# Kernel optimization log

Measured on AMD Instinct MI355X. Metric: run time of the kernel, lower is better.

## Reference

```python
import jax, jax.numpy as jnp
import numpy as np

GAMMA = 2.0
MARGIN = 0.3
SCALE = 30.0
B, C = 4096, 32768


def setup_inputs() -> dict:
    key = jax.random.key(0)
    k1, k2 = jax.random.split(key)
    inputs = jax.random.normal(k1, (B, C), dtype=jnp.float32)
    targets = jax.random.randint(k2, (B,), 0, C, dtype=jnp.int64)
    return {"inputs": inputs, "targets": targets}


def reference(inputs, targets):
    # Row-wise L2 normalize (F.normalize with eps=1e-12)
    norm = jnp.maximum(jnp.linalg.norm(inputs, axis=1, keepdims=True), 1e-12)
    normalized = inputs / norm  # (B, C)

    rows = jnp.arange(inputs.shape[0])
    # cos(theta) at target class
    cos_theta = normalized[rows, targets]
    theta = jnp.arccos(jnp.clip(cos_theta, -1.0 + 1e-7, 1.0 - 1e-7))
    cos_theta_m = jnp.cos(theta + MARGIN)

    # scatter margin-adjusted cosine back, then scale
    logits = normalized.at[rows, targets].set(cos_theta_m) * SCALE  # (B, C)

    # cross-entropy (no smoothing, no class weights)
    logp = jax.nn.log_softmax(logits, axis=1)
    ce = -logp[rows, targets]  # (B,)

    pt = jnp.exp(-ce)
    loss = (1.0 - pt) ** GAMMA * ce
    return jnp.mean(loss)
```

## Files before the change

### kernel.cpp

```cpp
#include <hip/hip_runtime.h>
#include <math.h>

#define B_ROWS 4096
#define C_COLS 32768
#define BLOCK  1024
#define NF4    (C_COLS / 4 / BLOCK)

typedef float v4f __attribute__((ext_vector_type(4)));

__device__ __forceinline__ float wave_reduce_sum(float v) {
    #pragma unroll
    for (int off = 32; off > 0; off >>= 1)
        v += __shfl_down(v, off, 64);
    return v;
}

__device__ __forceinline__ float block_reduce_sum(float v, float* red, int tid) {
    const int wid  = tid >> 6;
    const int lane = tid & 63;
    v = wave_reduce_sum(v);
    if (lane == 0) red[wid] = v;
    __syncthreads();
    if (wid == 0) {
        float s = (lane < 16) ? red[lane] : 0.0f;
        #pragma unroll
        for (int off = 8; off > 0; off >>= 1)
            s += __shfl_down(s, off, 64);
        if (lane == 0) red[0] = s;
    }
    __syncthreads();
    return red[0];
}

__global__ __launch_bounds__(BLOCK, 8)
void focal_row_kernel(const float* __restrict__ inp,
                      const int*   __restrict__ tgt,
                      float*       __restrict__ row_loss) {
    constexpr float SCALE = 30.0f;
    constexpr float COSM  = 0.9553364891f;
    constexpr float SINM  = 0.2955202067f;

    const int row = blockIdx.x;
    const int tid = threadIdx.x;

    const v4f* __restrict__ rowp = (const v4f*)(inp + (size_t)row * C_COLS);

    __shared__ float red_a[16];
    __shared__ float red_b[16];

    float xt = 0.0f;
    if (tid == 0) {
        const int ct = tgt[row];
        xt = inp[(size_t)row * C_COLS + ct];
    }

    v4f r[NF4];
    #pragma unroll
    for (int k = 0; k < NF4; ++k)
        r[k] = __builtin_nontemporal_load(rowp + (k * BLOCK + tid));

    float sumsq = 0.0f;
    #pragma unroll
    for (int k = 0; k < NF4; ++k) {
        sumsq = fmaf(r[k].x, r[k].x, sumsq);
        sumsq = fmaf(r[k].y, r[k].y, sumsq);
        sumsq = fmaf(r[k].z, r[k].z, sumsq);
        sumsq = fmaf(r[k].w, r[k].w, sumsq);
    }

    const float total_sq = block_reduce_sum(sumsq, red_a, tid);
    const float norm = fmaxf(sqrtf(total_sq), 1e-12f);
    const float inv  = SCALE / norm;

    float se = 0.0f;
    #pragma unroll
    for (int k = 0; k < NF4; ++k) {
        se += __expf(r[k].x * inv);
        se += __expf(r[k].y * inv);
        se += __expf(r[k].z * inv);
        se += __expf(r[k].w * inv);
    }
    const float sumexp_full = block_reduce_sum(se, red_b, tid);

    if (tid == 0) {
        const float c  = xt / norm;
        const float cc = fminf(fmaxf(c, -1.0f + 1e-7f), 1.0f - 1e-7f);
        const float sin_t = sqrtf(fmaxf(1.0f - cc * cc, 0.0f));
        const float cosm  = cc * COSM - sin_t * SINM;
        const float lt    = SCALE * cosm;

        const float Z  = sumexp_full - __expf(SCALE * c) + __expf(lt);
        const float ce = logf(Z) - lt;
        const float pt = __expf(-ce);
        const float om = 1.0f - pt;
        row_loss[row] = om * om * ce;
    }
}

__global__ __launch_bounds__(1024)
void finalize_kernel(const float* __restrict__ row_loss,
                     float*       __restrict__ out) {
    const int tid = threadIdx.x;
    __shared__ float red[16];
    float s = 0.0f;
    #pragma unroll
    for (int k = 0; k < B_ROWS / 1024; ++k)
        s += row_loss[k * 1024 + tid];
    const float total = block_reduce_sum(s, red, tid);
    if (tid == 0) out[0] = total * (1.0f / (float)B_ROWS);
}

extern "C" void kernel_launch(void* const* d_in, const int* in_sizes, int n_in,
                              void* d_out, int out_size, void* d_ws, size_t ws_size,
                              hipStream_t stream) {
    const float* inp = (const float*)d_in[0];
    const int*   tgt = (const int*)d_in[1];
    float*       out = (float*)d_out;
    float*       row_loss = (float*)d_ws;

    focal_row_kernel<<<B_ROWS, BLOCK, 0, stream>>>(inp, tgt, row_loss);
    finalize_kernel<<<1, 1024, 0, stream>>>(row_loss, out);
}
```

Measured before the change: 639.6 us.

## Make row kernel persistent with double-buffered next-row prefetch and LDS-only barriers

The grid shrinks to 256 blocks, and each block walks 16 consecutive rows. While the current row is reduced, the next row is loaded into a second register buffer. Barriers now wait only on LDS counters (lgkmcnt) rather than a full __syncthreads, so the in-flight global prefetch loads are not drained at each reduction. The aim is to hide memory latency behind the exp/reduction work and cut block launch overhead. The cost is lower occupancy (one 1024-thread block per CU with the launch bound relaxed to 4), higher register pressure, and dependence on a hand-encoded waitcnt value.

```diff
diff --git a/kernel.cpp b/kernel.cpp
--- a/kernel.cpp
+++ b/kernel.cpp
@@ -5,8 +5,15 @@
 #define C_COLS 32768
 #define BLOCK  1024
 #define NF4    (C_COLS / 4 / BLOCK)
+#define GRID   256
+#define RPB    (B_ROWS / GRID)
 
 typedef float v4f __attribute__((ext_vector_type(4)));
+
+__device__ __forceinline__ void bar_lds() {
+    __builtin_amdgcn_s_waitcnt(0xC07F);
+    __builtin_amdgcn_s_barrier();
+}
 
 __device__ __forceinline__ float wave_reduce_sum(float v) {
     #pragma unroll
@@ -20,7 +27,7 @@
     const int lane = tid & 63;
     v = wave_reduce_sum(v);
     if (lane == 0) red[wid] = v;
-    __syncthreads();
+    bar_lds();
     if (wid == 0) {
         float s = (lane < 16) ? red[lane] : 0.0f;
         #pragma unroll
@@ -28,11 +35,11 @@
             s += __shfl_down(s, off, 64);
         if (lane == 0) red[0] = s;
     }
-    __syncthreads();
+    bar_lds();
     return red[0];
 }
 
-__global__ __launch_bounds__(BLOCK, 8)
+__global__ __launch_bounds__(BLOCK, 4)
 void focal_row_kernel(const float* __restrict__ inp,
                       const int*   __restrict__ tgt,
                       float*       __restrict__ row_loss) {
@@ -40,60 +47,75 @@
     constexpr float COSM  = 0.9553364891f;
     constexpr float SINM  = 0.2955202067f;
 
-    const int row = blockIdx.x;
-    const int tid = threadIdx.x;
-
-    const v4f* __restrict__ rowp = (const v4f*)(inp + (size_t)row * C_COLS);
+    const int tid  = threadIdx.x;
+    const int row0 = blockIdx.x * RPB;
 
     __shared__ float red_a[16];
     __shared__ float red_b[16];
 
+    v4f buf[2][NF4];
+
+    {
+        const v4f* __restrict__ p = (const v4f*)(inp + (size_t)row0 * C_COLS);
+        #pragma unroll
+        for (int k = 0; k < NF4; ++k)
+            buf[0][k] = __builtin_nontemporal_load(p + (k * BLOCK + tid));
+    }
     float xt = 0.0f;
-    if (tid == 0) {
-        const int ct = tgt[row];
-        xt = inp[(size_t)row * C_COLS + ct];
-    }
+    if (tid == 0) xt = inp[(size_t)row0 * C_COLS + tgt[row0]];
 
-    v4f r[NF4];
-    #pragma unroll
-    for (int k = 0; k < NF4; ++k)
-        r[k] = __builtin_nontemporal_load(rowp + (k * BLOCK + tid));
+    #pragma unroll 2
+    for (int i = 0; i < RPB; ++i) {
+        const int row = row0 + i;
+        v4f* cur = buf[i & 1];
+        v4f* nxt = buf[(i + 1) & 1];
 
-    float sumsq = 0.0f;
-    #pragma unroll
-    for (int k = 0; k < NF4; ++k) {
-        sumsq = fmaf(r[k].x, r[k].x, sumsq);
-        sumsq = fmaf(r[k].y, r[k].y, sumsq);
-        sumsq = fmaf(r[k].z, r[k].z, sumsq);
-        sumsq = fmaf(r[k].w, r[k].w, sumsq);
-    }
+        float sumsq = 0.0f;
+        #pragma unroll
+        for (int k = 0; k < NF4; ++k) {
+            sumsq = fmaf(cur[k].x, cur[k].x, sumsq);
+            sumsq = fmaf(cur[k].y, cur[k].y, sumsq);
+            sumsq = fmaf(cur[k].z, cur[k].z, sumsq);
+            sumsq = fmaf(cur[k].w, cur[k].w, sumsq);
+        }
 
-    const float total_sq = block_reduce_sum(sumsq, red_a, tid);
-    const float norm = fmaxf(sqrtf(total_sq), 1e-12f);
-    const float inv  = SCALE / norm;
+        float xt_next = 0.0f;
+        if (i + 1 < RPB) {
+            const v4f* __restrict__ p = (const v4f*)(inp + (size_t)(row + 1) * C_COLS);
+            #pragma unroll
+            for (int k = 0; k < NF4; ++k)
+                nxt[k] = __builtin_nontemporal_load(p + (k * BLOCK + tid));
+            if (tid == 0) xt_next = inp[(size_t)(row + 1) * C_COLS + tgt[row + 1]];
+        }
 
-    float se = 0.0f;
-    #pragma unroll
-    for (int k = 0; k < NF4; ++k) {
-        se += __expf(r[k].x * inv);
-        se += __expf(r[k].y * inv);
-        se += __expf(r[k].z * inv);
-        se += __expf(r[k].w * inv);
-    }
-    const float sumexp_full = block_reduce_sum(se, red_b, tid);
+        const float total_sq = block_reduce_sum(sumsq, red_a, tid);
+        const float norm = fmaxf(sqrtf(total_sq), 1e-12f);
+        const float inv  = SCALE / norm;
 
-    if (tid == 0) {
-        const float c  = xt / norm;
-        const float cc = fminf(fmaxf(c, -1.0f + 1e-7f), 1.0f - 1e-7f);
-        const float sin_t = sqrtf(fmaxf(1.0f - cc * cc, 0.0f));
-        const float cosm  = cc * COSM - sin_t * SINM;
-        const float lt    = SCALE * cosm;
+        float se = 0.0f;
+        #pragma unroll
+        for (int k = 0; k < NF4; ++k) {
+            se += __expf(cur[k].x * inv);
+            se += __expf(cur[k].y * inv);
+            se += __expf(cur[k].z * inv);
+            se += __expf(cur[k].w * inv);
+        }
+        const float sumexp_full = block_reduce_sum(se, red_b, tid);
 
-        const float Z  = sumexp_full - __expf(SCALE * c) + __expf(lt);
-        const float ce = logf(Z) - lt;
-        const float pt = __expf(-ce);
-        const float om = 1.0f - pt;
-        row_loss[row] = om * om * ce;
+        if (tid == 0) {
+            const float c  = xt / norm;
+            const float cc = fminf(fmaxf(c, -1.0f + 1e-7f), 1.0f - 1e-7f);
+            const float sin_t = sqrtf(fmaxf(1.0f - cc * cc, 0.0f));
+            const float cosm  = cc * COSM - sin_t * SINM;
+            const float lt    = SCALE * cosm;
+
+            const float Z  = sumexp_full - __expf(SCALE * c) + __expf(lt);
+            const float ce = logf(Z) - lt;
+            const float pt = __expf(-ce);
+            const float om = 1.0f - pt;
+            row_loss[row] = om * om * ce;
+        }
+        xt = xt_next;
     }
 }
 
@@ -118,6 +140,6 @@
     float*       out = (float*)d_out;
     float*       row_loss = (float*)d_ws;
 
-    focal_row_kernel<<<B_ROWS, BLOCK, 0, stream>>>(inp, tgt, row_loss);
+    focal_row_kernel<<<GRID, BLOCK, 0, stream>>>(inp, tgt, row_loss);
     finalize_kernel<<<1, 1024, 0, stream>>>(row_loss, out);
 }
```

After: 658.7 us. +3.0%, slower.
